# Performance work log

Hardware: AMD Instinct MI355X
Metric: run time of the kernel (lower is better)

## Reference

```python
import jax, jax.numpy as jnp
import numpy as np

N = 16384      # tokens (batch*seq)
D = 2048       # input_size / d_model
E = 64         # num_experts
K = 2          # top_k
EPS = 1e-12    # F.normalize eps


def setup_inputs() -> dict:
    key = jax.random.key(0)
    k1, k2 = jax.random.split(key)
    x = jax.random.normal(k1, (N, D), dtype=jnp.float32)
    # nn.Linear(input_size, num_experts, bias=False) weight has shape [E, D]
    W = jax.random.normal(k2, (E, D), dtype=jnp.float32) / np.sqrt(D)
    return {"x": x, "W": W}


def reference(x, W):
    # router logits: [N, E], computed (and kept) in float32 as in .float()
    logits = jnp.matmul(x, W.T).astype(jnp.float32)

    top_k_logits, top_k_indices = jax.lax.top_k(logits, K)      # [N, K]
    top_k_gates = jax.nn.softmax(top_k_logits, axis=1).astype(x.dtype)

    # ---- training-mode aux loss ----
    probs = jax.nn.softmax(logits, axis=1)                      # [N, E]
    rows = jnp.arange(logits.shape[0])[:, None]                 # [N, 1]
    gates = jnp.zeros_like(probs).astype(top_k_gates.dtype)
    gates = gates.at[rows, top_k_indices].set(top_k_gates)      # dense [N, E]

    count = logits.shape[0]
    p_sum = probs.sum(axis=0)                                   # [E]
    freq = (gates > 0).astype(jnp.float32).sum(axis=0)          # [E]
    lse = jax.nn.logsumexp(logits, axis=-1)                     # [N]
    lsesq = jnp.sum(lse ** 2)

    p_norm = p_sum / jnp.maximum(jnp.sum(jnp.abs(p_sum)), EPS)   # L1 normalize
    f_norm = freq / jnp.maximum(jnp.sum(jnp.abs(freq)), EPS)
    switchloss = E * jnp.sum(p_norm * f_norm)
    z_loss = lsesq / count
    loss = switchloss + 0.1 * z_loss

    return top_k_indices, top_k_gates, loss
```

## Files before the change

### kernel.cpp

```cpp
#include <hip/hip_runtime.h>
#include <hip/hip_bf16.h>
#include <math.h>

#define N_TOK 16384
#define D_DIM 2048
#define E_EXP 64
#define KQ    256
#define NCHW  8
#define NBLK  256

typedef __attribute__((ext_vector_type(8))) short bf16x8;
typedef __attribute__((ext_vector_type(16))) float f32x16;
typedef __attribute__((ext_vector_type(4))) unsigned int u32x4;

#define PACK2(HI, LO) __builtin_amdgcn_perm((HI), (LO), 0x07060302u)

typedef union { unsigned u[4]; bf16x8 v; } b8u;

__global__ void pack_w(const float* __restrict__ W,
                       unsigned short* __restrict__ Wp) {
  const int T = blockIdx.x * 256 + threadIdx.x;
  const int e = T & 63, j = (T >> 6) & 3, c = T >> 8;
  const float* src = W + (size_t)e * D_DIM + c * 32 + j * 8;
  float4 v0 = *(const float4*)src;
  float4 v1 = *(const float4*)(src + 4);
  float vv[8] = {v0.x, v0.y, v0.z, v0.w, v1.x, v1.y, v1.z, v1.w};
  unsigned hu[8], mu[8], lu[8];
#pragma unroll
  for (int q = 0; q < 8; ++q) {
    unsigned u = __float_as_uint(vv[q]);
    unsigned a = u & 0xffff0000u;
    float r = vv[q] - __uint_as_float(a);
    unsigned b = __float_as_uint(r) & 0xffff0000u;
    float r2 = r - __uint_as_float(b);
    unsigned d = __float_as_uint(r2) & 0xffff0000u;
    hu[q] = a; mu[q] = b; lu[q] = d;
  }
  u32x4 ph, pm, pl;
#pragma unroll
  for (int q = 0; q < 4; ++q) {
    ph[q] = PACK2(hu[2 * q + 1], hu[2 * q]);
    pm[q] = PACK2(mu[2 * q + 1], mu[2 * q]);
    pl[q] = PACK2(lu[2 * q + 1], lu[2 * q]);
  }
  const size_t base = (size_t)c * 6144 + (j >> 1) * 3072 + (j & 1) * 512 + e * 8;
  *(u32x4*)(Wp + base)        = ph;
  *(u32x4*)(Wp + base + 1024) = pm;
  *(u32x4*)(Wp + base + 2048) = pl;
}

struct XS { float4 a0, a1, b0, b1, c0, c1, d0, d1; };

__global__ __launch_bounds__(512)
void fused_router(const float* __restrict__ x,
                  const unsigned short* __restrict__ Wp,
                  float* __restrict__ out,
                  double* __restrict__ blk_ps,
                  double* __restrict__ blk_z,
                  unsigned* __restrict__ freq) {
  __shared__ float s_c[2][64][66];
  __shared__ float s_m[64], s_inv[64];
  __shared__ unsigned hist[64];
  const int tid  = threadIdx.x;
  const int lane = tid & 63;
  const int kq   = tid >> 6;
  const int T0   = blockIdx.x * 64;
  if (tid < 64) hist[tid] = 0u;

  const int r  = lane & 31;
  const int kg = lane >> 5;
  const float* xg0 = x + (size_t)(T0 + r) * D_DIM + kq * KQ + kg * 8;
  const float* xg1 = xg0 + (size_t)32 * D_DIM;
  const unsigned short* bp =
      Wp + (size_t)(kq * NCHW) * 6144 + kg * 512 + r * 8;

  f32x16 acc00 = (f32x16)0.f, acc01 = (f32x16)0.f;
  f32x16 acc10 = (f32x16)0.f, acc11 = (f32x16)0.f;

#define CVT8(V0, V1, OH, OM, OL)                                            \
  do {                                                                      \
    float vv[8] = {(V0).x, (V0).y, (V0).z, (V0).w,                          \
                   (V1).x, (V1).y, (V1).z, (V1).w};                         \
    unsigned hu[8], mu[8], lu[8];                                           \
    _Pragma("unroll") for (int q = 0; q < 8; ++q) {                         \
      unsigned u = __float_as_uint(vv[q]);                                  \
      unsigned a = u & 0xffff0000u;                                         \
      float rr = vv[q] - __uint_as_float(a);                                \
      unsigned b = __float_as_uint(rr) & 0xffff0000u;                       \
      float r2 = rr - __uint_as_float(b);                                   \
      unsigned d = __float_as_uint(r2) & 0xffff0000u;                       \
      hu[q] = a; mu[q] = b; lu[q] = d;                                      \
    }                                                                       \
    b8u th, tm, tl;                                                         \
    _Pragma("unroll") for (int q = 0; q < 4; ++q) {                         \
      th.u[q] = PACK2(hu[2 * q + 1], hu[2 * q]);                            \
      tm.u[q] = PACK2(mu[2 * q + 1], mu[2 * q]);                            \
      tl.u[q] = PACK2(lu[2 * q + 1], lu[2 * q]);                            \
    }                                                                       \
    OH = th.v; OM = tm.v; OL = tl.v;                                        \
  } while (0)

#define MM6(AH, AM, AL, BH, BM, BL, ACC)                                      \
    ACC = __builtin_amdgcn_mfma_f32_32x32x16_bf16(AH, BH, ACC, 0, 0, 0);      \
    ACC = __builtin_amdgcn_mfma_f32_32x32x16_bf16(AH, BM, ACC, 0, 0, 0);      \
    ACC = __builtin_amdgcn_mfma_f32_32x32x16_bf16(AM, BH, ACC, 0, 0, 0);      \
    ACC = __builtin_amdgcn_mfma_f32_32x32x16_bf16(AH, BL, ACC, 0, 0, 0);      \
    ACC = __builtin_amdgcn_mfma_f32_32x32x16_bf16(AM, BM, ACC, 0, 0, 0);      \
    ACC = __builtin_amdgcn_mfma_f32_32x32x16_bf16(AL, BH, ACC, 0, 0, 0)

#define LOADX(S, C)                                                         \
  do {                                                                      \
    const float* p0_ = xg0 + (C) * 32;                                      \
    const float* p1_ = xg1 + (C) * 32;                                      \
    S.a0 = *(const float4*)(p0_);      S.a1 = *(const float4*)(p0_ + 4);    \
    S.b0 = *(const float4*)(p0_ + 16); S.b1 = *(const float4*)(p0_ + 20);   \
    S.c0 = *(const float4*)(p1_);      S.c1 = *(const float4*)(p1_ + 4);    \
    S.d0 = *(const float4*)(p1_ + 16); S.d1 = *(const float4*)(p1_ + 20);   \
  } while (0)

#define BODY(C, XU, XN, DOPRE)                                              \
  {                                                                         \
    const unsigned short* bc = bp + (size_t)(C) * 6144;                     \
    bf16x8 B00h = *(const bf16x8*)(bc);                                     \
    bf16x8 B00m = *(const bf16x8*)(bc + 1024);                              \
    bf16x8 B00l = *(const bf16x8*)(bc + 2048);                              \
    bf16x8 B01h = *(const bf16x8*)(bc + 256);                               \
    bf16x8 B01m = *(const bf16x8*)(bc + 256 + 1024);                        \
    bf16x8 B01l = *(const bf16x8*)(bc + 256 + 2048);                        \
    bf16x8 B10h = *(const bf16x8*)(bc + 3072);                              \
    bf16x8 B10m = *(const bf16x8*)(bc + 3072 + 1024);                       \
    bf16x8 B10l = *(const bf16x8*)(bc + 3072 + 2048);                       \
    bf16x8 B11h = *(const bf16x8*)(bc + 3072 + 256);                        \
    bf16x8 B11m = *(const bf16x8*)(bc + 3072 + 256 + 1024);                 \
    bf16x8 B11l = *(const bf16x8*)(bc + 3072 + 256 + 2048);                 \
    if (DOPRE) LOADX(XN, (C) + 1);     \
    {                                                                       \
      bf16x8 A0h, A0m, A0l, A1h, A1m, A1l;                                  \
      CVT8(XU.a0, XU.a1, A0h, A0m, A0l);            \
      CVT8(XU.b0, XU.b1, A1h, A1m, A1l);            \
      MM6(A0h, A0m, A0l, B00h, B00m, B00l, acc00);                          \
      MM6(A0h, A0m, A0l, B01h, B01m, B01l, acc01);                          \
      MM6(A1h, A1m, A1l, B10h, B10m, B10l, acc00);                          \
      MM6(A1h, A1m, A1l, B11h, B11m, B11l, acc01);                          \
    }                                                                       \
    {                                                                       \
      bf16x8 A0h, A0m, A0l, A1h, A1m, A1l;                                  \
      CVT8(XU.c0, XU.c1, A0h, A0m, A0l);           \
      CVT8(XU.d0, XU.d1, A1h, A1m, A1l);           \
      MM6(A0h, A0m, A0l, B00h, B00m, B00l, acc10);                          \
      MM6(A0h, A0m, A0l, B01h, B01m, B01l, acc11);                          \
      MM6(A1h, A1m, A1l, B10h, B10m, B10l, acc10);                          \
      MM6(A1h, A1m, A1l, B11h, B11m, B11l, acc11);                          \
    }                                                                       \
  }

  XS xA, xB;
  LOADX(xA, 0);
#pragma unroll
  for (int cc = 0; cc < NCHW; cc += 2) {
    BODY(cc, xA, xB, (cc + 1) < NCHW);
    BODY(cc + 1, xB, xA, (cc + 2) < NCHW);
  }
#undef BODY
#undef LOADX
#undef MM6
#undef CVT8

  const int slot = kq & 1;
#define SCAT(OP)                                                            \
  _Pragma("unroll") for (int reg = 0; reg < 16; ++reg) {                    \
    const int tl_ = (reg & 3) + 8 * (reg >> 2) + 4 * kg;                    \
    s_c[slot][tl_][r]           OP acc00[reg];                              \
    s_c[slot][tl_][32 + r]      OP acc01[reg];                              \
    s_c[slot][32 + tl_][r]      OP acc10[reg];                              \
    s_c[slot][32 + tl_][32 + r] OP acc11[reg];                              \
  }
  if (kq < 2) SCAT(=);
  __syncthreads();
  if (kq == 2 || kq == 3) SCAT(+=);
  __syncthreads();
  if (kq == 4 || kq == 5) SCAT(+=);
  __syncthreads();
  if (kq == 6 || kq == 7) SCAT(+=);
  __syncthreads();
#undef SCAT
  {
    const int t = tid >> 3, e0 = (tid & 7) * 8;
#pragma unroll
    for (int q = 0; q < 8; ++q)
      s_c[0][t][e0 + q] += s_c[1][t][e0 + q];
  }
  __syncthreads();

  if (tid < 64) {
    const int t = tid;
    float m = -3.402823466e38f;
#pragma unroll
    for (int e = 0; e < 64; ++e) m = fmaxf(m, s_c[0][t][e]);
    float sum = 0.f;
#pragma unroll
    for (int e = 0; e < 64; ++e) sum += __expf(s_c[0][t][e] - m);
    const float lse = m + __logf(sum);
    const float inv = 1.0f / sum;
    s_m[t] = m;
    s_inv[t] = inv;

    float v0 = s_c[0][t][0], v1 = -3.402823466e38f;
    int i0 = 0, i1 = 0;
#pragma unroll
    for (int e = 1; e < 64; ++e) {
      float le = s_c[0][t][e];
      bool g0 = le > v0;
      bool g1 = le > v1;
      float nv1 = g0 ? v0 : (g1 ? le : v1);
      int   ni1 = g0 ? i0 : (g1 ? e  : i1);
      v0 = g0 ? le : v0;
      i0 = g0 ? e  : i0;
      v1 = nv1; i1 = ni1;
    }
    float dd = __expf(v1 - v0);
    float g0 = 1.0f / (1.0f + dd);
    float g1 = dd * g0;

    const int tg = T0 + t;
    out[tg * 2 + 0] = (float)i0;
    out[tg * 2 + 1] = (float)i1;
    out[2 * N_TOK + tg * 2 + 0] = g0;
    out[2 * N_TOK + tg * 2 + 1] = g1;

    atomicAdd(&hist[i0], 1u);
    atomicAdd(&hist[i1], 1u);

    float z = lse * lse;
    z += __shfl_xor(z, 32, 64);
    z += __shfl_xor(z, 16, 64);
    z += __shfl_xor(z, 8, 64);
    z += __shfl_xor(z, 4, 64);
    z += __shfl_xor(z, 2, 64);
    z += __shfl_xor(z, 1, 64);
    if (tid == 0) blk_z[blockIdx.x] = (double)z;
  }
  __syncthreads();

  if (tid >= 64 && tid < 128) {
    const int e = tid - 64;
    float cs2 = 0.f;
#pragma unroll 8
    for (int t = 0; t < 64; ++t)
      cs2 += __expf(s_c[0][t][e] - s_m[t]) * s_inv[t];
    blk_ps[(size_t)blockIdx.x * 64 + e] = (double)cs2;
  }
  if (tid < 64 && hist[tid]) atomicAdd(&freq[tid], hist[tid]);
}

__global__ void finalize(const double* __restrict__ blk_ps,
                         const double* __restrict__ blk_z,
                         const unsigned* __restrict__ freq,
                         float* __restrict__ out_loss) {
  const int lane = threadIdx.x;
  double p = 0.0;
  for (int b = 0; b < NBLK; ++b) p += blk_ps[(size_t)b * 64 + lane];
  double zt = 0.0;
#pragma unroll
  for (int b = 0; b < NBLK / 64; ++b) zt += blk_z[lane * (NBLK / 64) + b];
#pragma unroll
  for (int off = 32; off >= 1; off >>= 1) zt += __shfl_xor(zt, off, 64);

  double f = (double)freq[lane];
  double pa = fabs(p);
  double fa = fabs(f);
#pragma unroll
  for (int off = 32; off >= 1; off >>= 1) {
    pa += __shfl_xor(pa, off, 64);
    fa += __shfl_xor(fa, off, 64);
  }
  pa = pa > 1e-12 ? pa : 1e-12;
  fa = fa > 1e-12 ? fa : 1e-12;

  double s = (p / pa) * (f / fa);
#pragma unroll
  for (int off = 32; off >= 1; off >>= 1) s += __shfl_xor(s, off, 64);

  if (lane == 0) {
    double switchloss = 64.0 * s;
    double z_loss = zt / (double)N_TOK;
    out_loss[0] = (float)(switchloss + 0.1 * z_loss);
  }
}

extern "C" void kernel_launch(void* const* d_in, const int* in_sizes, int n_in,
                              void* d_out, int out_size, void* d_ws, size_t ws_size,
                              hipStream_t stream) {
  const float* x = (const float*)d_in[0];
  const float* W = (const float*)d_in[1];
  float* out = (float*)d_out;

  double* blk_ps = (double*)d_ws;
  double* blk_z  = blk_ps + NBLK * 64;
  unsigned* freq = (unsigned*)(blk_z + NBLK);
  size_t woff = (NBLK * 64 * 8 + NBLK * 8 + 64 * 4 + 255) & ~(size_t)255;
  unsigned short* Wp = (unsigned short*)((char*)d_ws + woff);

  hipMemsetAsync(freq, 0, 64 * sizeof(unsigned), stream);

  pack_w<<<64, 256, 0, stream>>>(W, Wp);
  fused_router<<<NBLK, 512, 0, stream>>>(x, Wp, out, blk_ps, blk_z, freq);
  finalize<<<1, 64, 0, stream>>>(blk_ps, blk_z, freq, out + 4 * N_TOK);
}
```

Baseline: 56.94 us.

## Restructure K-loop into finer 16-wide steps with double-buffered x and W prefetch

The inner reduction loop now walks 16 smaller k-steps instead of 8 larger chunks. Each step holds half the x data and half the W fragments in a staging struct, and two stages are double-buffered so the W loads are prefetched one step ahead together with x. Previously W was loaded at the start of each chunk with no prefetch. The aim is to hide global-load latency for W behind MFMA work and to lower peak register use per stage, at the cost of more loop iterations and smaller load batches.

```diff
diff --git a/kernel.cpp b/kernel.cpp
--- a/kernel.cpp
+++ b/kernel.cpp
@@ -6,7 +6,7 @@
 #define D_DIM 2048
 #define E_EXP 64
 #define KQ    256
-#define NCHW  8
+#define NKS   16
 #define NBLK  256
 
 typedef __attribute__((ext_vector_type(8))) short bf16x8;
@@ -49,7 +49,10 @@
   *(u32x4*)(Wp + base + 2048) = pl;
 }
 
-struct XS { float4 a0, a1, b0, b1, c0, c1, d0, d1; };
+struct KSst {
+  float4 a0, a1, c0, c1;
+  bf16x8 B0h, B0m, B0l, B1h, B1m, B1l;
+};
 
 __global__ __launch_bounds__(512)
 void fused_router(const float* __restrict__ x,
@@ -69,10 +72,9 @@
 
   const int r  = lane & 31;
   const int kg = lane >> 5;
-  const float* xg0 = x + (size_t)(T0 + r) * D_DIM + kq * KQ + kg * 8;
-  const float* xg1 = xg0 + (size_t)32 * D_DIM;
-  const unsigned short* bp =
-      Wp + (size_t)(kq * NCHW) * 6144 + kg * 512 + r * 8;
+  const float* xa = x + (size_t)(T0 + r) * D_DIM + kq * KQ + kg * 8;
+  const float* xc = xa + (size_t)32 * D_DIM;
+  const unsigned short* bq = Wp + (size_t)(kq * 8) * 6144 + kg * 512 + r * 8;
 
   f32x16 acc00 = (f32x16)0.f, acc01 = (f32x16)0.f;
   f32x16 acc10 = (f32x16)0.f, acc11 = (f32x16)0.f;
@@ -108,61 +110,47 @@
     ACC = __builtin_amdgcn_mfma_f32_32x32x16_bf16(AM, BM, ACC, 0, 0, 0);      \
     ACC = __builtin_amdgcn_mfma_f32_32x32x16_bf16(AL, BH, ACC, 0, 0, 0)
 
-#define LOADX(S, C)                                                         \
+#define LOADS(S, KS)                                                        \
   do {                                                                      \
-    const float* p0_ = xg0 + (C) * 32;                                      \
-    const float* p1_ = xg1 + (C) * 32;                                      \
-    S.a0 = *(const float4*)(p0_);      S.a1 = *(const float4*)(p0_ + 4);    \
-    S.b0 = *(const float4*)(p0_ + 16); S.b1 = *(const float4*)(p0_ + 20);   \
-    S.c0 = *(const float4*)(p1_);      S.c1 = *(const float4*)(p1_ + 4);    \
-    S.d0 = *(const float4*)(p1_ + 16); S.d1 = *(const float4*)(p1_ + 20);   \
+    const float* xp_ = xa + (KS) * 16;                                      \
+    const float* xq_ = xc + (KS) * 16;                                      \
+    S.a0 = *(const float4*)(xp_);  S.a1 = *(const float4*)(xp_ + 4);        \
+    S.c0 = *(const float4*)(xq_);  S.c1 = *(const float4*)(xq_ + 4);        \
+    const unsigned short* bk_ = bq + (size_t)(KS) * 3072;                   \
+    S.B0h = *(const bf16x8*)(bk_);                                          \
+    S.B0m = *(const bf16x8*)(bk_ + 1024);                                   \
+    S.B0l = *(const bf16x8*)(bk_ + 2048);                                   \
+    S.B1h = *(const bf16x8*)(bk_ + 256);                                    \
+    S.B1m = *(const bf16x8*)(bk_ + 256 + 1024);                             \
+    S.B1l = *(const bf16x8*)(bk_ + 256 + 2048);                             \
   } while (0)
 
-#define BODY(C, XU, XN, DOPRE)                                              \
+#define CONSUME(S)                                                          \
   {                                                                         \
-    const unsigned short* bc = bp + (size_t)(C) * 6144;                     \
-    bf16x8 B00h = *(const bf16x8*)(bc);                                     \
-    bf16x8 B00m = *(const bf16x8*)(bc + 1024);                              \
-    bf16x8 B00l = *(const bf16x8*)(bc + 2048);                              \
-    bf16x8 B01h = *(const bf16x8*)(bc + 256);                               \
-    bf16x8 B01m = *(const bf16x8*)(bc + 256 + 1024);                        \
-    bf16x8 B01l = *(const bf16x8*)(bc + 256 + 2048);                        \
-    bf16x8 B10h = *(const bf16x8*)(bc + 3072);                              \
-    bf16x8 B10m = *(const bf16x8*)(bc + 3072 + 1024);                       \
-    bf16x8 B10l = *(const bf16x8*)(bc + 3072 + 2048);                       \
-    bf16x8 B11h = *(const bf16x8*)(bc + 3072 + 256);                        \
-    bf16x8 B11m = *(const bf16x8*)(bc + 3072 + 256 + 1024);                 \
-    bf16x8 B11l = *(const bf16x8*)(bc + 3072 + 256 + 2048);                 \
-    if (DOPRE) LOADX(XN, (C) + 1);     \
-    {                                                                       \
-      bf16x8 A0h, A0m, A0l, A1h, A1m, A1l;                                  \
-      CVT8(XU.a0, XU.a1, A0h, A0m, A0l);            \
-      CVT8(XU.b0, XU.b1, A1h, A1m, A1l);            \
-      MM6(A0h, A0m, A0l, B00h, B00m, B00l, acc00);                          \
-      MM6(A0h, A0m, A0l, B01h, B01m, B01l, acc01);                          \
-      MM6(A1h, A1m, A1l, B10h, B10m, B10l, acc00);                          \
-      MM6(A1h, A1m, A1l, B11h, B11m, B11l, acc01);                          \
-    }                                                                       \
-    {                                                                       \
-      bf16x8 A0h, A0m, A0l, A1h, A1m, A1l;                                  \
-      CVT8(XU.c0, XU.c1, A0h, A0m, A0l);           \
-      CVT8(XU.d0, XU.d1, A1h, A1m, A1l);           \
-      MM6(A0h, A0m, A0l, B00h, B00m, B00l, acc10);                          \
-      MM6(A0h, A0m, A0l, B01h, B01m, B01l, acc11);                          \
-      MM6(A1h, A1m, A1l, B10h, B10m, B10l, acc10);                          \
-      MM6(A1h, A1m, A1l, B11h, B11m, B11l, acc11);                          \
-    }                                                                       \
-  }
-
-  XS xA, xB;
-  LOADX(xA, 0);
-#pragma unroll
-  for (int cc = 0; cc < NCHW; cc += 2) {
-    BODY(cc, xA, xB, (cc + 1) < NCHW);
-    BODY(cc + 1, xB, xA, (cc + 2) < NCHW);
-  }
-#undef BODY
-#undef LOADX
+    bf16x8 Ah, Am, Al;                                                      \
+    CVT8(S.a0, S.a1, Ah, Am, Al);                                           \
+    MM6(Ah, Am, Al, S.B0h, S.B0m, S.B0l, acc00);                            \
+    MM6(Ah, Am, Al, S.B1h, S.B1m, S.B1l, acc01);                            \
+  }                                                                         \
+  {                                                                         \
+    bf16x8 Ch, Cm, Cl;                                                      \
+    CVT8(S.c0, S.c1, Ch, Cm, Cl);                                           \
+    MM6(Ch, Cm, Cl, S.B0h, S.B0m, S.B0l, acc10);                            \
+    MM6(Ch, Cm, Cl, S.B1h, S.B1m, S.B1l, acc11);                            \
+  }
+
+  KSst S0, S1;
+  LOADS(S0, 0);
+  LOADS(S1, 1);
+#pragma unroll
+  for (int ks = 0; ks < NKS; ks += 2) {
+    CONSUME(S0);
+    if (ks + 2 < NKS) LOADS(S0, ks + 2);
+    CONSUME(S1);
+    if (ks + 3 < NKS) LOADS(S1, ks + 3);
+  }
+#undef CONSUME
+#undef LOADS
 #undef MM6
 #undef CVT8
 
```

Result: slower. 59.26 us (+4.1%).
